# Kernel tuning notes

Measured on AMD Instinct MI355X. Metric: run time of the kernel, lower is better.

Reference implementation:

```python
import jax, jax.numpy as jnp
import numpy as np

B, H, W, C = 4, 180, 320, 64
ATTN_SCALE = 0.125  # C ** -0.5
EPS = 1e-6  # flax LayerNorm default epsilon


def _layer_norm(x, scale, bias):
    mu = jnp.mean(x, axis=-1, keepdims=True)
    var = jnp.mean(jnp.square(x - mu), axis=-1, keepdims=True)
    return (x - mu) * jax.lax.rsqrt(var + EPS) * scale + bias


def setup_inputs() -> dict:
    key = jax.random.key(0)
    ks = jax.random.split(key, 8)
    w_init = 1.0 / np.sqrt(C)  # lecun_normal-ish scale for CxC dense kernels
    return {
        "x_l": jax.random.normal(ks[0], (B, H, W, C), jnp.float32),
        "x_r": jax.random.normal(ks[1], (B, H, W, C), jnp.float32),
        "ln_l_scale": jnp.ones((C,), jnp.float32),
        "ln_l_bias": jnp.zeros((C,), jnp.float32),
        "ln_r_scale": jnp.ones((C,), jnp.float32),
        "ln_r_bias": jnp.zeros((C,), jnp.float32),
        "w_ql": jax.random.normal(ks[2], (C, C), jnp.float32) * w_init,
        "b_ql": jnp.zeros((C,), jnp.float32),
        "w_qr": jax.random.normal(ks[3], (C, C), jnp.float32) * w_init,
        "b_qr": jnp.zeros((C,), jnp.float32),
        "w_vl": jax.random.normal(ks[4], (C, C), jnp.float32) * w_init,
        "b_vl": jnp.zeros((C,), jnp.float32),
        "w_vr": jax.random.normal(ks[5], (C, C), jnp.float32) * w_init,
        "b_vr": jnp.zeros((C,), jnp.float32),
        "beta": jax.random.normal(ks[6], (1, 1, 1, C), jnp.float32) * 0.1,
        "gamma": jax.random.normal(ks[7], (1, 1, 1, C), jnp.float32) * 0.1,
    }


def reference(x_l, x_r, ln_l_scale, ln_l_bias, ln_r_scale, ln_r_bias,
              w_ql, b_ql, w_qr, b_qr, w_vl, b_vl, w_vr, b_vr, beta, gamma):
    # Projections (attention runs along the width axis, per (b, h) scanline)
    q_l = _layer_norm(x_l, ln_l_scale, ln_l_bias) @ w_ql + b_ql   # [B,H,W,C]
    q_r = _layer_norm(x_r, ln_r_scale, ln_r_bias) @ w_qr + b_qr   # [B,H,W,C]
    v_l = x_l @ w_vl + b_vl                                       # [B,H,W,C]
    v_r = x_r @ w_vr + b_vr                                       # [B,H,W,C]

    # Shared score matrix: [B, H, W_l, W_r]
    attn = jnp.einsum('bhlc,bhrc->bhlr', q_l, q_r) * ATTN_SCALE

    # Row softmax (over W_r) attends right->left
    f_r2l = jnp.einsum('bhlr,bhrc->bhlc', jax.nn.softmax(attn, axis=-1), v_r) * beta
    # Column softmax (over W_l) attends left->right
    f_l2r = jnp.einsum('bhlr,bhlc->bhrc', jax.nn.softmax(attn, axis=-2), v_l) * gamma

    return (x_l + f_r2l, x_r + f_l2r)
```

## Files before the change

kernel.cpp:

```cpp
#include <hip/hip_runtime.h>
#include <hip/hip_bf16.h>

#define NB 4
#define NH 180
#define NW 320
#define NC 64
#define NSCAN (NB*NH)
#define NROWS (NB*NH*NW)
#define NELEM ((size_t)NROWS*NC)

using short8  = __attribute__((ext_vector_type(8))) short;
using floatx4 = __attribute__((ext_vector_type(4))) float;

__device__ __forceinline__ float bflo(unsigned int u) { return __uint_as_float(u << 16); }
__device__ __forceinline__ float bfhi(unsigned int u) { return __uint_as_float(u & 0xffff0000u); }

__device__ __forceinline__ unsigned short fbf(float f) {
    __hip_bfloat16 h = __float2bfloat16(f);
    unsigned short s; __builtin_memcpy(&s, &h, 2); return s;
}
__device__ __forceinline__ unsigned int packbf(float lo, float hi) {
    return (unsigned int)fbf(lo) | ((unsigned int)fbf(hi) << 16);
}

#define SCALE_LOG2E 0.18033688011112042f

__global__ __launch_bounds__(256) void proj_kernel(
    const float* __restrict__ xl, const float* __restrict__ xr,
    const float* __restrict__ lsl, const float* __restrict__ lbl,
    const float* __restrict__ lsr, const float* __restrict__ lbr,
    const float* __restrict__ wql, const float* __restrict__ bql,
    const float* __restrict__ wqr, const float* __restrict__ bqr,
    const float* __restrict__ wvl, const float* __restrict__ bvl,
    const float* __restrict__ wvr, const float* __restrict__ bvr,
    __hip_bfloat16* __restrict__ ql, __hip_bfloat16* __restrict__ qr,
    __hip_bfloat16* __restrict__ vlT, __hip_bfloat16* __restrict__ vrT)
{
    const int p    = blockIdx.y;
    const int t    = threadIdx.x;
    const int row0 = blockIdx.x * 256;

    const float* src  = (p == 0 || p == 2) ? xl : xr;
    const float* Wm   = (p == 0) ? wql : (p == 1) ? wqr : (p == 2) ? wvl : wvr;
    const float* bias = (p == 0) ? bql : (p == 1) ? bqr : (p == 2) ? bvl : bvr;
    __hip_bfloat16* dst = (p == 0) ? ql : (p == 1) ? qr : (p == 2) ? vlT : vrT;
    const bool doLN = (p < 2);
    const float* lns = (p == 0) ? lsl : lsr;
    const float* lnb = (p == 0) ? lbl : lbr;

    __shared__ __align__(16) __hip_bfloat16 sA[256 * 72];
    __shared__ __align__(16) __hip_bfloat16 sWt[64 * 72];
    __shared__ float sLs[64], sLb[64], sBias[64];

    if (t < 64) {
        sLs[t]   = doLN ? lns[t] : 1.0f;
        sLb[t]   = doLN ? lnb[t] : 0.0f;
        sBias[t] = bias[t];
    }
    {
        const int k  = t >> 2;
        const int c0 = (t & 3) * 16;
        const float4* wrow = (const float4*)(Wm + k * NC + c0);
        float wv[16];
#pragma unroll
        for (int j = 0; j < 4; ++j) {
            float4 w4 = wrow[j];
            wv[4*j] = w4.x; wv[4*j+1] = w4.y; wv[4*j+2] = w4.z; wv[4*j+3] = w4.w;
        }
#pragma unroll
        for (int j = 0; j < 16; ++j)
            sWt[(c0 + j) * 72 + k] = __float2bfloat16(wv[j]);
    }
    __syncthreads();

    {
        const float4* x4 = (const float4*)(src + (size_t)(row0 + t) * NC);
        float f[64];
#pragma unroll
        for (int j = 0; j < 16; ++j) {
            float4 v = x4[j];
            f[4*j] = v.x; f[4*j+1] = v.y; f[4*j+2] = v.z; f[4*j+3] = v.w;
        }
        if (doLN) {
            float s = 0.f, s2 = 0.f;
#pragma unroll
            for (int c = 0; c < 64; ++c) { s += f[c]; s2 = fmaf(f[c], f[c], s2); }
            const float mu   = s * (1.0f / 64.0f);
            const float var  = s2 * (1.0f / 64.0f) - mu * mu;
            const float rstd = rsqrtf(var + 1e-6f);
#pragma unroll
            for (int c = 0; c < 64; ++c) f[c] = (f[c] - mu) * rstd * sLs[c] + sLb[c];
        }
        unsigned int* arow = (unsigned int*)&sA[t * 72];
#pragma unroll
        for (int j = 0; j < 32; ++j) arow[j] = packbf(f[2*j], f[2*j+1]);
    }
    __syncthreads();

    const int lane = t & 63;
    const int wv_  = t >> 6;
    const int quad = lane >> 4;
    const int mn   = lane & 15;

    short8 bfr[4][2];
#pragma unroll
    for (int nt = 0; nt < 4; ++nt)
#pragma unroll
        for (int ks = 0; ks < 2; ++ks)
            bfr[nt][ks] = *(const short8*)&sWt[(nt * 16 + mn) * 72 + ks * 32 + quad * 8];

#pragma unroll
    for (int mt = 0; mt < 4; ++mt) {
        const int rl = wv_ * 64 + mt * 16 + mn;
        short8 a0 = *(const short8*)&sA[rl * 72 +      quad * 8];
        short8 a1 = *(const short8*)&sA[rl * 72 + 32 + quad * 8];
#pragma unroll
        for (int nt = 0; nt < 4; ++nt) {
            floatx4 c = {0.f, 0.f, 0.f, 0.f};
            c = __builtin_amdgcn_mfma_f32_16x16x32_bf16(a0, bfr[nt][0], c, 0, 0, 0);
            c = __builtin_amdgcn_mfma_f32_16x16x32_bf16(a1, bfr[nt][1], c, 0, 0, 0);
            const int col = nt * 16 + mn;
            const float bb = sBias[col];
            if (p < 2) {
#pragma unroll
                for (int i = 0; i < 4; ++i) {
                    const int rowl = wv_ * 64 + mt * 16 + quad * 4 + i;
                    dst[(size_t)(row0 + rowl) * NC + col] = __float2bfloat16(c[i] + bb);
                }
            } else {
#pragma unroll
                for (int i = 0; i < 4; ++i) {
                    const unsigned grow = (unsigned)(row0 + wv_ * 64 + mt * 16 + quad * 4 + i);
                    const unsigned sc   = grow / 320u;
                    const unsigned wr   = grow - sc * 320u;
                    dst[(size_t)sc * (NC * NW) + (unsigned)col * NW + wr] =
                        __float2bfloat16(c[i] + bb);
                }
            }
        }
    }
}

__global__ __launch_bounds__(256) void attn_kernel(
    const __hip_bfloat16* __restrict__ ql, const __hip_bfloat16* __restrict__ qr,
    const __hip_bfloat16* __restrict__ vlT, const __hip_bfloat16* __restrict__ vrT,
    const float* __restrict__ xl, const float* __restrict__ xr,
    const float* __restrict__ beta, const float* __restrict__ gamma,
    float* __restrict__ out)
{
    const int mt   = blockIdx.x;
    const int scan = blockIdx.y;
    const int p    = blockIdx.z;
    const int t    = threadIdx.x;
    const int lane = t & 63;
    const int w    = t >> 6;
    const int quad = lane >> 4;
    const int mn   = lane & 15;
    const int m0   = mt * 64;

    const __hip_bfloat16* Q  = (p ? qr  : ql ) + (size_t)scan * (NW * NC);
    const __hip_bfloat16* K  = (p ? ql  : qr ) + (size_t)scan * (NW * NC);
    const __hip_bfloat16* VT = (p ? vlT : vrT) + (size_t)scan * (NC * NW);
    const float* xS = p ? xr : xl;
    const float* gv = p ? gamma : beta;

    __shared__ __align__(16) __hip_bfloat16 sQ[64 * 72];
    __shared__ __align__(16) __hip_bfloat16 sP[64 * 72];
    __shared__ __align__(16) char sU[18432];
    __shared__ float sRS[64];
    __hip_bfloat16* sK  = (__hip_bfloat16*)sU;
    __hip_bfloat16* sVt = (__hip_bfloat16*)(sU + 9216);
    float* sO = (float*)sU;

    {
        const int r = t >> 2, c0 = (t & 3) * 16;
        const uint4* g = (const uint4*)(Q + (size_t)(m0 + r) * NC + c0);
        uint4 a = g[0], b = g[1];
        uint4* d = (uint4*)&sQ[r * 72 + c0];
        d[0] = a; d[1] = b;
    }
    __syncthreads();

    const short8 qa0 = *(const short8*)&sQ[(w * 16 + mn) * 72 +      quad * 8];
    const short8 qa1 = *(const short8*)&sQ[(w * 16 + mn) * 72 + 32 + quad * 8];

    floatx4 acc[4];
#pragma unroll
    for (int nt = 0; nt < 4; ++nt) acc[nt] = (floatx4){0.f, 0.f, 0.f, 0.f};
    float rs = 0.f;

    for (int rb = 0; rb < NW; rb += 64) {
        __syncthreads();
        {
            const int r = t >> 2, c0 = (t & 3) * 16;
            const uint4* gk = (const uint4*)(K + (size_t)(rb + r) * NC + c0);
            uint4 a = gk[0], b = gk[1];
            const uint4* gt = (const uint4*)(VT + (size_t)r * NW + rb + c0);
            uint4 cc = gt[0], d = gt[1];
            uint4* dk = (uint4*)&sK [r * 72 + c0]; dk[0] = a;  dk[1] = b;
            uint4* dv = (uint4*)&sVt[r * 72 + c0]; dv[0] = cc; dv[1] = d;
        }
        __syncthreads();

#pragma unroll
        for (int rt = 0; rt < 4; ++rt) {
            short8 b0 = *(const short8*)&sK[(rt * 16 + mn) * 72 +      quad * 8];
            short8 b1 = *(const short8*)&sK[(rt * 16 + mn) * 72 + 32 + quad * 8];
            floatx4 s = {0.f, 0.f, 0.f, 0.f};
            s = __builtin_amdgcn_mfma_f32_16x16x32_bf16(qa0, b0, s, 0, 0, 0);
            s = __builtin_amdgcn_mfma_f32_16x16x32_bf16(qa1, b1, s, 0, 0, 0);
#pragma unroll
            for (int i = 0; i < 4; ++i) {
                const float wgt = exp2f(s[i] * SCALE_LOG2E);
                sP[(w * 16 + quad * 4 + i) * 72 + rt * 16 + mn] = __float2bfloat16(wgt);
            }
        }

#pragma unroll
        for (int ks = 0; ks < 2; ++ks) {
            short8 pa = *(const short8*)&sP[(w * 16 + mn) * 72 + ks * 32 + quad * 8];
#pragma unroll
            for (int nt = 0; nt < 4; ++nt) {
                short8 vb = *(const short8*)&sVt[(nt * 16 + mn) * 72 + ks * 32 + quad * 8];
                acc[nt] = __builtin_amdgcn_mfma_f32_16x16x32_bf16(pa, vb, acc[nt], 0, 0, 0);
            }
        }

        {
            const uint4* pr = (const uint4*)&sP[(w * 16 + mn) * 72 + quad * 16];
            uint4 a = pr[0], b = pr[1];
            float s = bflo(a.x) + bfhi(a.x) + bflo(a.y) + bfhi(a.y)
                    + bflo(a.z) + bfhi(a.z) + bflo(a.w) + bfhi(a.w)
                    + bflo(b.x) + bfhi(b.x) + bflo(b.y) + bfhi(b.y)
                    + bflo(b.z) + bfhi(b.z) + bflo(b.w) + bfhi(b.w);
            s += __shfl_xor(s, 16);
            s += __shfl_xor(s, 32);
            rs += s;
        }
    }

    __syncthreads();

    if (lane < 16) sRS[w * 16 + lane] = 1.0f / rs;
#pragma unroll
    for (int nt = 0; nt < 4; ++nt)
#pragma unroll
        for (int i = 0; i < 4; ++i)
            sO[(w * 16 + quad * 4 + i) * 68 + nt * 16 + mn] = acc[nt][i];
    __syncthreads();

    {
        const int m = t >> 2, c0 = (t & 3) * 16;
        const float inv = sRS[m];
        const int grow = scan * NW + m0 + m;
        const float4* xg = (const float4*)(xS + (size_t)grow * NC + c0);
        const float4* gg = (const float4*)(gv + c0);
        const float4* so = (const float4*)&sO[m * 68 + c0];
        float4* og = (float4*)(out + (p ? NELEM : (size_t)0) + (size_t)grow * NC + c0);
#pragma unroll
        for (int j = 0; j < 4; ++j) {
            float4 xv = xg[j];
            float4 gvv = gg[j];
            float4 ov = so[j];
            float4 o;
            o.x = xv.x + ov.x * inv * gvv.x;
            o.y = xv.y + ov.y * inv * gvv.y;
            o.z = xv.z + ov.z * inv * gvv.z;
            o.w = xv.w + ov.w * inv * gvv.w;
            og[j] = o;
        }
    }
}

extern "C" void kernel_launch(void* const* d_in, const int* in_sizes, int n_in,
                              void* d_out, int out_size, void* d_ws, size_t ws_size,
                              hipStream_t stream)
{
    const float* xl  = (const float*)d_in[0];
    const float* xr  = (const float*)d_in[1];
    const float* lsl = (const float*)d_in[2];
    const float* lbl = (const float*)d_in[3];
    const float* lsr = (const float*)d_in[4];
    const float* lbr = (const float*)d_in[5];
    const float* wql = (const float*)d_in[6];
    const float* bql = (const float*)d_in[7];
    const float* wqr = (const float*)d_in[8];
    const float* bqr = (const float*)d_in[9];
    const float* wvl = (const float*)d_in[10];
    const float* bvl = (const float*)d_in[11];
    const float* wvr = (const float*)d_in[12];
    const float* bvr = (const float*)d_in[13];
    const float* beta  = (const float*)d_in[14];
    const float* gamma = (const float*)d_in[15];

    __hip_bfloat16* ws   = (__hip_bfloat16*)d_ws;
    __hip_bfloat16* ql_  = ws;
    __hip_bfloat16* qr_  = ws + NELEM;
    __hip_bfloat16* vlT_ = ws + 2 * NELEM;
    __hip_bfloat16* vrT_ = ws + 3 * NELEM;

    proj_kernel<<<dim3(NROWS / 256, 4, 1), 256, 0, stream>>>(
        xl, xr, lsl, lbl, lsr, lbr, wql, bql, wqr, bqr, wvl, bvl, wvr, bvr,
        ql_, qr_, vlT_, vrT_);

    attn_kernel<<<dim3(5, NSCAN, 2), 256, 0, stream>>>(
        ql_, qr_, vlT_, vrT_, xl, xr, beta, gamma, (float*)d_out);
}
```

Before: 391.5 us.

## Prefetch K/V tiles into registers, transpose score MFMA, fold softmax scale into q_l

The attention kernel now loads the next K and V^T tile into registers while computing on the current one, so global-load latency overlaps with MFMA work. It swaps the MFMA operands so each lane holds a score row slice, packs the bf16 exp weights straight into shared memory, and keeps the row-sum in registers instead of re-reading the P tile. Q and P share one shared buffer, s_setprio is raised around the compute, and blocks are remapped across XCDs. The softmax scale is folded into the q_l projection output. The exp2 without a scale multiply relies on the exponent being premultiplied, which only holds for the p=0 operand; p=1 blocks use ql as K, which also carries the scale, so the product is scaled correctly either way.

```diff
diff --git a/kernel.cpp b/kernel.cpp
--- a/kernel.cpp
+++ b/kernel.cpp
@@ -47,6 +47,7 @@
     const bool doLN = (p < 2);
     const float* lns = (p == 0) ? lsl : lsr;
     const float* lnb = (p == 0) ? lbl : lbr;
+    const float oscale = (p == 0) ? SCALE_LOG2E : 1.0f;
 
     __shared__ __align__(16) __hip_bfloat16 sA[256 * 72];
     __shared__ __align__(16) __hip_bfloat16 sWt[64 * 72];
@@ -125,7 +126,8 @@
 #pragma unroll
                 for (int i = 0; i < 4; ++i) {
                     const int rowl = wv_ * 64 + mt * 16 + quad * 4 + i;
-                    dst[(size_t)(row0 + rowl) * NC + col] = __float2bfloat16(c[i] + bb);
+                    dst[(size_t)(row0 + rowl) * NC + col] =
+                        __float2bfloat16((c[i] + bb) * oscale);
                 }
             } else {
 #pragma unroll
@@ -148,9 +150,13 @@
     const float* __restrict__ beta, const float* __restrict__ gamma,
     float* __restrict__ out)
 {
-    const int mt   = blockIdx.x;
-    const int scan = blockIdx.y;
-    const int p    = blockIdx.z;
+    const int flat = blockIdx.x + 5 * (blockIdx.y + 720 * blockIdx.z);
+    const int g    = (flat & 7) * 900 + (flat >> 3);
+    const int mt   = g % 5;
+    const int s2   = g / 5;
+    const int p    = s2 & 1;
+    const int scan = s2 >> 1;
+
     const int t    = threadIdx.x;
     const int lane = t & 63;
     const int w    = t >> 6;
@@ -164,25 +170,34 @@
     const float* xS = p ? xr : xl;
     const float* gv = p ? gamma : beta;
 
-    __shared__ __align__(16) __hip_bfloat16 sQ[64 * 72];
-    __shared__ __align__(16) __hip_bfloat16 sP[64 * 72];
+    __shared__ __align__(16) __hip_bfloat16 sQP[64 * 72];
     __shared__ __align__(16) char sU[18432];
     __shared__ float sRS[64];
     __hip_bfloat16* sK  = (__hip_bfloat16*)sU;
     __hip_bfloat16* sVt = (__hip_bfloat16*)(sU + 9216);
     float* sO = (float*)sU;
 
-    {
-        const int r = t >> 2, c0 = (t & 3) * 16;
-        const uint4* g = (const uint4*)(Q + (size_t)(m0 + r) * NC + c0);
-        uint4 a = g[0], b = g[1];
-        uint4* d = (uint4*)&sQ[r * 72 + c0];
+    const int sr  = t >> 2;
+    const int sc0 = (t & 3) * 16;
+
+    uint4 rk0, rk1, rv0, rv1;
+    {
+        const uint4* gk = (const uint4*)(K + (size_t)sr * NC + sc0);
+        rk0 = gk[0]; rk1 = gk[1];
+        const uint4* gt = (const uint4*)(VT + (size_t)sr * NW + sc0);
+        rv0 = gt[0]; rv1 = gt[1];
+    }
+
+    {
+        const uint4* gq = (const uint4*)(Q + (size_t)(m0 + sr) * NC + sc0);
+        uint4 a = gq[0], b = gq[1];
+        uint4* d = (uint4*)&sQP[sr * 72 + sc0];
         d[0] = a; d[1] = b;
     }
     __syncthreads();
 
-    const short8 qa0 = *(const short8*)&sQ[(w * 16 + mn) * 72 +      quad * 8];
-    const short8 qa1 = *(const short8*)&sQ[(w * 16 + mn) * 72 + 32 + quad * 8];
+    const short8 qa0 = *(const short8*)&sQP[(w * 16 + mn) * 72 +      quad * 8];
+    const short8 qa1 = *(const short8*)&sQP[(w * 16 + mn) * 72 + 32 + quad * 8];
 
     floatx4 acc[4];
 #pragma unroll
@@ -192,52 +207,47 @@
     for (int rb = 0; rb < NW; rb += 64) {
         __syncthreads();
         {
-            const int r = t >> 2, c0 = (t & 3) * 16;
-            const uint4* gk = (const uint4*)(K + (size_t)(rb + r) * NC + c0);
-            uint4 a = gk[0], b = gk[1];
-            const uint4* gt = (const uint4*)(VT + (size_t)r * NW + rb + c0);
-            uint4 cc = gt[0], d = gt[1];
-            uint4* dk = (uint4*)&sK [r * 72 + c0]; dk[0] = a;  dk[1] = b;
-            uint4* dv = (uint4*)&sVt[r * 72 + c0]; dv[0] = cc; dv[1] = d;
+            uint4* dk = (uint4*)&sK [sr * 72 + sc0]; dk[0] = rk0; dk[1] = rk1;
+            uint4* dv = (uint4*)&sVt[sr * 72 + sc0]; dv[0] = rv0; dv[1] = rv1;
         }
         __syncthreads();
 
+        if (rb + 64 < NW) {
+            const uint4* gk = (const uint4*)(K + (size_t)(rb + 64 + sr) * NC + sc0);
+            rk0 = gk[0]; rk1 = gk[1];
+            const uint4* gt = (const uint4*)(VT + (size_t)sr * NW + (rb + 64) + sc0);
+            rv0 = gt[0]; rv1 = gt[1];
+        }
+
+        __builtin_amdgcn_s_setprio(1);
 #pragma unroll
         for (int rt = 0; rt < 4; ++rt) {
-            short8 b0 = *(const short8*)&sK[(rt * 16 + mn) * 72 +      quad * 8];
-            short8 b1 = *(const short8*)&sK[(rt * 16 + mn) * 72 + 32 + quad * 8];
+            short8 ka0 = *(const short8*)&sK[(rt * 16 + mn) * 72 +      quad * 8];
+            short8 ka1 = *(const short8*)&sK[(rt * 16 + mn) * 72 + 32 + quad * 8];
             floatx4 s = {0.f, 0.f, 0.f, 0.f};
-            s = __builtin_amdgcn_mfma_f32_16x16x32_bf16(qa0, b0, s, 0, 0, 0);
-            s = __builtin_amdgcn_mfma_f32_16x16x32_bf16(qa1, b1, s, 0, 0, 0);
-#pragma unroll
-            for (int i = 0; i < 4; ++i) {
-                const float wgt = exp2f(s[i] * SCALE_LOG2E);
-                sP[(w * 16 + quad * 4 + i) * 72 + rt * 16 + mn] = __float2bfloat16(wgt);
-            }
+            s = __builtin_amdgcn_mfma_f32_16x16x32_bf16(ka0, qa0, s, 0, 0, 0);
+            s = __builtin_amdgcn_mfma_f32_16x16x32_bf16(ka1, qa1, s, 0, 0, 0);
+            const unsigned c0 = packbf(exp2f(s[0]), exp2f(s[1]));
+            const unsigned c1 = packbf(exp2f(s[2]), exp2f(s[3]));
+            rs += bflo(c0) + bfhi(c0) + bflo(c1) + bfhi(c1);
+            uint2 pk; pk.x = c0; pk.y = c1;
+            *(uint2*)&sQP[(w * 16 + mn) * 72 + rt * 16 + quad * 4] = pk;
         }
 
 #pragma unroll
         for (int ks = 0; ks < 2; ++ks) {
-            short8 pa = *(const short8*)&sP[(w * 16 + mn) * 72 + ks * 32 + quad * 8];
+            short8 pa = *(const short8*)&sQP[(w * 16 + mn) * 72 + ks * 32 + quad * 8];
 #pragma unroll
             for (int nt = 0; nt < 4; ++nt) {
                 short8 vb = *(const short8*)&sVt[(nt * 16 + mn) * 72 + ks * 32 + quad * 8];
                 acc[nt] = __builtin_amdgcn_mfma_f32_16x16x32_bf16(pa, vb, acc[nt], 0, 0, 0);
             }
         }
-
-        {
-            const uint4* pr = (const uint4*)&sP[(w * 16 + mn) * 72 + quad * 16];
-            uint4 a = pr[0], b = pr[1];
-            float s = bflo(a.x) + bfhi(a.x) + bflo(a.y) + bfhi(a.y)
-                    + bflo(a.z) + bfhi(a.z) + bflo(a.w) + bfhi(a.w)
-                    + bflo(b.x) + bfhi(b.x) + bflo(b.y) + bfhi(b.y)
-                    + bflo(b.z) + bfhi(b.z) + bflo(b.w) + bfhi(b.w);
-            s += __shfl_xor(s, 16);
-            s += __shfl_xor(s, 32);
-            rs += s;
-        }
-    }
+        __builtin_amdgcn_s_setprio(0);
+    }
+
+    rs += __shfl_xor(rs, 16);
+    rs += __shfl_xor(rs, 32);
 
     __syncthreads();
 
```

New measurement: 375.0 us. -4.2%, faster.
